# Kernel optimization log

Measured on AMD Instinct MI355X. Metric: run time of the kernel, lower is better.

## Reference

```python
import jax, jax.numpy as jnp
import numpy as np

B, N, F_IN, F_OUT = 16, 4096, 64, 64


def setup_inputs() -> dict:
    key = jax.random.key(0)
    k1, k2, k3, k4 = jax.random.split(key, 4)
    stdv = 1.0 / np.sqrt(F_OUT)
    graph = jax.random.normal(k1, (B, N, F_IN), dtype=jnp.float32)
    adj = jax.random.uniform(k2, (N, N), dtype=jnp.float32)
    weight = jax.random.uniform(k3, (F_IN, F_OUT), minval=-stdv, maxval=stdv, dtype=jnp.float32)
    bias = jax.random.uniform(k4, (F_OUT,), minval=-stdv, maxval=stdv, dtype=jnp.float32)
    return {"graph": graph, "adj": adj, "weight": weight, "bias": bias}


def _normalize_adj(adj):
    # Symmetric normalization D^{-1/2} A D^{-1/2}.
    # diag_embed @ adj @ diag_embed == row/col elementwise scaling (same math, O(N^2)).
    rowsum = jnp.sum(adj, axis=-1)
    rowsum = rowsum + (rowsum == 0).astype(adj.dtype)  # avoid div-by-zero for isolated nodes
    d_inv_sqrt = rowsum ** -0.5
    return d_inv_sqrt[:, None] * adj * d_inv_sqrt[None, :]


def reference(graph, adj, weight, bias):
    adj_norm = _normalize_adj(adj)                      # [N, N]
    support = jnp.einsum('bni,io->bno', graph, weight)  # [B, N, F_out]
    output = jnp.einsum('nm,bmo->bno', adj_norm, support)
    output = jax.nn.relu(output + bias)
    return (output, adj)
```

## Files before the change

kernel.cpp:

```cpp
#include <hip/hip_runtime.h>
#include <hip/hip_bf16.h>
#include <stdint.h>


typedef __bf16 bf16;
typedef __bf16 bf16x8 __attribute__((ext_vector_type(8)));
typedef float f32x4 __attribute__((ext_vector_type(4)));

#define NN 4096
#define BATCH 16
#define FD 64

__global__ __launch_bounds__(256) void k_prep(const float* __restrict__ adj,
                                              bf16* __restrict__ adjb,
                                              float* __restrict__ dsq) {
    int row = blockIdx.x;
    const float4* p = (const float4*)(adj + (size_t)row * NN);
    uint4* q = (uint4*)(adjb + (size_t)row * NN);
    float s = 0.f;
    for (int j = threadIdx.x; j < 512; j += 256) {
        float4 a = p[2 * j], b = p[2 * j + 1];
        bf16x8 h;
        h[0] = (bf16)a.x; h[1] = (bf16)a.y; h[2] = (bf16)a.z; h[3] = (bf16)a.w;
        h[4] = (bf16)b.x; h[5] = (bf16)b.y; h[6] = (bf16)b.z; h[7] = (bf16)b.w;
        q[j] = __builtin_bit_cast(uint4, h);
        s += a.x + a.y + a.z + a.w + b.x + b.y + b.z + b.w;
    }
    #pragma unroll
    for (int off = 32; off > 0; off >>= 1) s += __shfl_down(s, off, 64);
    __shared__ float red[4];
    int lane = threadIdx.x & 63, wv = threadIdx.x >> 6;
    if (lane == 0) red[wv] = s;
    __syncthreads();
    if (threadIdx.x == 0) {
        float t = red[0] + red[1] + red[2] + red[3];
        if (t == 0.f) t = 1.f;
        dsq[row] = 1.0f / sqrtf(t);
    }
}

__global__ __launch_bounds__(256) void k_support(const float* __restrict__ graph,
                                                 const float* __restrict__ weight,
                                                 const float* __restrict__ dsq,
                                                 bf16* __restrict__ spT) {
    __shared__ float wT[64 * 64];
    int tid = threadIdx.x;
    for (int idx = tid; idx < 4096; idx += 256) {
        int i = idx >> 6, o = idx & 63;
        wT[o * 64 + i] = weight[idx];
    }
    __syncthreads();
    int b = blockIdx.y;
    int m = blockIdx.x * 256 + tid;
    const float4* g4 = (const float4*)(graph + ((size_t)b * NN + m) * FD);
    float ds = dsq[m];
    float gr[64];
    #pragma unroll
    for (int j = 0; j < 16; j++) {
        float4 v = g4[j];
        gr[4 * j] = v.x * ds; gr[4 * j + 1] = v.y * ds;
        gr[4 * j + 2] = v.z * ds; gr[4 * j + 3] = v.w * ds;
    }
    bf16* outp = spT + m;
    for (int o = 0; o < 64; o++) {
        const float4* w4 = (const float4*)&wT[o * 64];
        float acc = 0.f;
        #pragma unroll
        for (int j = 0; j < 16; j++) {
            float4 wv = w4[j];
            acc += gr[4 * j] * wv.x + gr[4 * j + 1] * wv.y
                 + gr[4 * j + 2] * wv.z + gr[4 * j + 3] * wv.w;
        }
        outp[(size_t)(b * 64 + o) * NN] = (bf16)acc;
    }
}

__global__ __launch_bounds__(256) void k_gemm(const bf16* __restrict__ adjb,
                                              const bf16* __restrict__ spT,
                                              const float* __restrict__ dsq,
                                              const float* __restrict__ bias,
                                              float* __restrict__ out) {
    __shared__ uint4 lds_a[512];
    __shared__ uint4 lds_b[512];
    const int tid = threadIdx.x;
    const int lane = tid & 63;
    const int w = tid >> 6;
    const int n0 = blockIdx.x * 128;
    const int c0 = blockIdx.y * 128;

    const int q0 = tid, q1 = tid + 256;
    const uint4* pA0 = (const uint4*)(adjb + (size_t)(n0 + (q0 >> 2)) * NN) + (q0 & 3);
    const uint4* pA1 = (const uint4*)(adjb + (size_t)(n0 + (q1 >> 2)) * NN) + (q1 & 3);
    const uint4* pB0 = (const uint4*)(spT  + (size_t)(c0 + (q0 >> 2)) * NN) + (q0 & 3);
    const uint4* pB1 = (const uint4*)(spT  + (size_t)(c0 + (q1 >> 2)) * NN) + (q1 & 3);

    const int r = lane & 15, qo = lane >> 4;
    const int rm = (w >> 1) * 64, rc = (w & 1) * 64;
    const bf16x8* fA = (const bf16x8*)lds_a + (rm + r) * 4 + qo;
    const bf16x8* fB = (const bf16x8*)lds_b + (rc + r) * 4 + qo;

    f32x4 acc[4][4];
    #pragma unroll
    for (int i = 0; i < 4; i++)
        #pragma unroll
        for (int j = 0; j < 4; j++)
            acc[i][j] = (f32x4){0.f, 0.f, 0.f, 0.f};

    for (int kt = 0; kt < NN; kt += 32) {
        const int kd = kt >> 3;
        uint4 va0 = pA0[kd], va1 = pA1[kd];
        uint4 vb0 = pB0[kd], vb1 = pB1[kd];
        __syncthreads();
        lds_a[q0] = va0; lds_a[q1] = va1;
        lds_b[q0] = vb0; lds_b[q1] = vb1;
        __syncthreads();
        bf16x8 af[4], bfr[4];
        #pragma unroll
        for (int mi = 0; mi < 4; mi++) af[mi] = fA[mi * 64];
        #pragma unroll
        for (int ni = 0; ni < 4; ni++) bfr[ni] = fB[ni * 64];
        #pragma unroll
        for (int mi = 0; mi < 4; mi++)
            #pragma unroll
            for (int ni = 0; ni < 4; ni++)
                acc[mi][ni] = __builtin_amdgcn_mfma_f32_16x16x32_bf16(
                    af[mi], bfr[ni], acc[mi][ni], 0, 0, 0);
    }

    const int b_hi = (c0 + rc) >> 6;
    float* outp = out + (size_t)b_hi * (NN * FD);
    float bo[4];
    #pragma unroll
    for (int ni = 0; ni < 4; ni++) bo[ni] = bias[ni * 16 + r];
    #pragma unroll
    for (int mi = 0; mi < 4; mi++) {
        float dn[4];
        #pragma unroll
        for (int rr = 0; rr < 4; rr++) dn[rr] = dsq[n0 + rm + mi * 16 + qo * 4 + rr];
        #pragma unroll
        for (int ni = 0; ni < 4; ni++) {
            int o = ni * 16 + r;
            #pragma unroll
            for (int rr = 0; rr < 4; rr++) {
                int n = n0 + rm + mi * 16 + qo * 4 + rr;
                float v = fmaxf(dn[rr] * acc[mi][ni][rr] + bo[ni], 0.f);
                outp[(size_t)n * FD + o] = v;
            }
        }
    }
}

__global__ __launch_bounds__(256) void k_copy(const float4* __restrict__ src,
                                              float4* __restrict__ dst) {
    size_t i = (size_t)blockIdx.x * 256 + threadIdx.x;
    dst[i] = src[i];
}

extern "C" void kernel_launch(void* const* d_in, const int* in_sizes, int n_in,
                              void* d_out, int out_size, void* d_ws, size_t ws_size,
                              hipStream_t stream) {
    const float *graph = nullptr, *adj = nullptr, *weight = nullptr, *bias = nullptr;
    for (int i = 0; i < n_in; i++) {
        const float* p = (const float*)d_in[i];
        switch (in_sizes[i]) {
            case BATCH * NN * FD: graph  = p; break;
            case NN * NN:         adj    = p; break;
            case FD * FD:         weight = p; break;
            case FD:              bias   = p; break;
        }
    }

    float* out0 = (float*)d_out;
    float* out1 = out0 + (size_t)BATCH * NN * FD;

    const size_t off_spT = (size_t)NN * NN * 2;
    const size_t off_dsq = off_spT + (size_t)1024 * NN * 2;
    const size_t need    = off_dsq + (size_t)NN * 4;
    char* scratch = (ws_size >= need) ? (char*)d_ws : (char*)out1;
    bf16*  adjb = (bf16*)scratch;
    bf16*  spT  = (bf16*)(scratch + off_spT);
    float* dsq  = (float*)(scratch + off_dsq);

    hipLaunchKernelGGL(k_prep, dim3(NN), dim3(256), 0, stream, adj, adjb, dsq);
    hipLaunchKernelGGL(k_support, dim3(16, 16), dim3(256), 0, stream,
                       graph, weight, dsq, spT);
    hipLaunchKernelGGL(k_gemm, dim3(32, 8), dim3(256), 0, stream,
                       adjb, spT, dsq, bias, out0);
    hipLaunchKernelGGL(k_copy, dim3(16384), dim3(256), 0, stream,
                       (const float4*)adj, (float4*)out1);
}
```

Before: 266.8 us.

## Split-K GEMM with atomic accumulation, swizzled LDS, and fused adj copy

Splits the adjacency GEMM along K into 4 chunks. This raises the grid from 256 to 1024 blocks so the GPU's CUs are better filled, and each chunk's partials are added into a zeroed fp32 scratch buffer with atomics. A separate epilogue kernel then applies degree scaling, bias and ReLU. It also XOR-swizzles the LDS layout to cut bank conflicts, and folds the adj passthrough copy and accumulator zeroing into the prep kernel so the separate copy pass is skipped when workspace is available. The cost is 16MB of extra scratch traffic, atomic contention, and results that depend on the order of the atomic float adds.

```diff
diff --git a/kernel.cpp b/kernel.cpp
--- a/kernel.cpp
+++ b/kernel.cpp
@@ -10,22 +10,33 @@
 #define NN 4096
 #define BATCH 16
 #define FD 64
+#define CDIM 1024
+
+__device__ __forceinline__ int swz(int q) {
+    return (q & ~3) | ((q & 3) ^ ((q >> 3) & 3));
+}
 
 __global__ __launch_bounds__(256) void k_prep(const float* __restrict__ adj,
                                               bf16* __restrict__ adjb,
-                                              float* __restrict__ dsq) {
+                                              float* __restrict__ dsq,
+                                              float4* __restrict__ acc4,
+                                              float4* __restrict__ out1,
+                                              int do_copy) {
     int row = blockIdx.x;
     const float4* p = (const float4*)(adj + (size_t)row * NN);
     uint4* q = (uint4*)(adjb + (size_t)row * NN);
+    float4* o = out1 + (size_t)row * (NN / 4);
     float s = 0.f;
     for (int j = threadIdx.x; j < 512; j += 256) {
         float4 a = p[2 * j], b = p[2 * j + 1];
+        if (do_copy) { o[2 * j] = a; o[2 * j + 1] = b; }
         bf16x8 h;
         h[0] = (bf16)a.x; h[1] = (bf16)a.y; h[2] = (bf16)a.z; h[3] = (bf16)a.w;
         h[4] = (bf16)b.x; h[5] = (bf16)b.y; h[6] = (bf16)b.z; h[7] = (bf16)b.w;
         q[j] = __builtin_bit_cast(uint4, h);
         s += a.x + a.y + a.z + a.w + b.x + b.y + b.z + b.w;
     }
+    acc4[(size_t)row * 256 + threadIdx.x] = (float4){0.f, 0.f, 0.f, 0.f};
     #pragma unroll
     for (int off = 32; off > 0; off >>= 1) s += __shfl_down(s, off, 64);
     __shared__ float red[4];
@@ -77,9 +88,7 @@
 
 __global__ __launch_bounds__(256) void k_gemm(const bf16* __restrict__ adjb,
                                               const bf16* __restrict__ spT,
-                                              const float* __restrict__ dsq,
-                                              const float* __restrict__ bias,
-                                              float* __restrict__ out) {
+                                              float* __restrict__ accb) {
     __shared__ uint4 lds_a[512];
     __shared__ uint4 lds_b[512];
     const int tid = threadIdx.x;
@@ -87,32 +96,34 @@
     const int w = tid >> 6;
     const int n0 = blockIdx.x * 128;
     const int c0 = blockIdx.y * 128;
+    const size_t kbase = (size_t)blockIdx.z * (NN / 4);
 
     const int q0 = tid, q1 = tid + 256;
-    const uint4* pA0 = (const uint4*)(adjb + (size_t)(n0 + (q0 >> 2)) * NN) + (q0 & 3);
-    const uint4* pA1 = (const uint4*)(adjb + (size_t)(n0 + (q1 >> 2)) * NN) + (q1 & 3);
-    const uint4* pB0 = (const uint4*)(spT  + (size_t)(c0 + (q0 >> 2)) * NN) + (q0 & 3);
-    const uint4* pB1 = (const uint4*)(spT  + (size_t)(c0 + (q1 >> 2)) * NN) + (q1 & 3);
+    const int w0 = swz(q0), w1 = swz(q1);
+    const uint4* pA0 = (const uint4*)(adjb + (size_t)(n0 + (q0 >> 2)) * NN + kbase) + (q0 & 3);
+    const uint4* pA1 = (const uint4*)(adjb + (size_t)(n0 + (q1 >> 2)) * NN + kbase) + (q1 & 3);
+    const uint4* pB0 = (const uint4*)(spT  + (size_t)(c0 + (q0 >> 2)) * NN + kbase) + (q0 & 3);
+    const uint4* pB1 = (const uint4*)(spT  + (size_t)(c0 + (q1 >> 2)) * NN + kbase) + (q1 & 3);
 
     const int r = lane & 15, qo = lane >> 4;
     const int rm = (w >> 1) * 64, rc = (w & 1) * 64;
-    const bf16x8* fA = (const bf16x8*)lds_a + (rm + r) * 4 + qo;
-    const bf16x8* fB = (const bf16x8*)lds_b + (rc + r) * 4 + qo;
-
-    f32x4 acc[4][4];
+    const bf16x8* fA = (const bf16x8*)lds_a + (rm + r) * 4 + (qo ^ (((rm + r) >> 1) & 3));
+    const bf16x8* fB = (const bf16x8*)lds_b + (rc + r) * 4 + (qo ^ (((rc + r) >> 1) & 3));
+
+    f32x4 ac[4][4];
     #pragma unroll
     for (int i = 0; i < 4; i++)
         #pragma unroll
         for (int j = 0; j < 4; j++)
-            acc[i][j] = (f32x4){0.f, 0.f, 0.f, 0.f};
-
-    for (int kt = 0; kt < NN; kt += 32) {
+            ac[i][j] = (f32x4){0.f, 0.f, 0.f, 0.f};
+
+    for (int kt = 0; kt < NN / 4; kt += 32) {
         const int kd = kt >> 3;
         uint4 va0 = pA0[kd], va1 = pA1[kd];
         uint4 vb0 = pB0[kd], vb1 = pB1[kd];
         __syncthreads();
-        lds_a[q0] = va0; lds_a[q1] = va1;
-        lds_b[q0] = vb0; lds_b[q1] = vb1;
+        lds_a[w0] = va0; lds_a[w1] = va1;
+        lds_b[w0] = vb0; lds_b[w1] = vb1;
         __syncthreads();
         bf16x8 af[4], bfr[4];
         #pragma unroll
@@ -123,31 +134,40 @@
         for (int mi = 0; mi < 4; mi++)
             #pragma unroll
             for (int ni = 0; ni < 4; ni++)
-                acc[mi][ni] = __builtin_amdgcn_mfma_f32_16x16x32_bf16(
-                    af[mi], bfr[ni], acc[mi][ni], 0, 0, 0);
-    }
-
-    const int b_hi = (c0 + rc) >> 6;
-    float* outp = out + (size_t)b_hi * (NN * FD);
-    float bo[4];
-    #pragma unroll
-    for (int ni = 0; ni < 4; ni++) bo[ni] = bias[ni * 16 + r];
-    #pragma unroll
-    for (int mi = 0; mi < 4; mi++) {
-        float dn[4];
-        #pragma unroll
-        for (int rr = 0; rr < 4; rr++) dn[rr] = dsq[n0 + rm + mi * 16 + qo * 4 + rr];
+                ac[mi][ni] = __builtin_amdgcn_mfma_f32_16x16x32_bf16(
+                    af[mi], bfr[ni], ac[mi][ni], 0, 0, 0);
+    }
+
+    #pragma unroll
+    for (int mi = 0; mi < 4; mi++)
         #pragma unroll
         for (int ni = 0; ni < 4; ni++) {
-            int o = ni * 16 + r;
+            int c = c0 + rc + ni * 16 + r;
             #pragma unroll
             for (int rr = 0; rr < 4; rr++) {
                 int n = n0 + rm + mi * 16 + qo * 4 + rr;
-                float v = fmaxf(dn[rr] * acc[mi][ni][rr] + bo[ni], 0.f);
-                outp[(size_t)n * FD + o] = v;
+                unsafeAtomicAdd(&accb[(size_t)n * CDIM + c], ac[mi][ni][rr]);
             }
         }
-    }
+}
+
+__global__ __launch_bounds__(256) void k_epi(const float4* __restrict__ accv,
+                                             const float* __restrict__ dsq,
+                                             const float* __restrict__ bias,
+                                             float4* __restrict__ out0) {
+    int idx = blockIdx.x * 256 + threadIdx.x;
+    int flat = idx * 4;
+    int o4 = flat & 63;
+    int n = (flat >> 6) & (NN - 1);
+    int b = flat >> 18;
+    float4 a = accv[((size_t)n * CDIM + b * 64 + o4) >> 2];
+    float d = dsq[n];
+    float4 r;
+    r.x = fmaxf(a.x * d + bias[o4 + 0], 0.f);
+    r.y = fmaxf(a.y * d + bias[o4 + 1], 0.f);
+    r.z = fmaxf(a.z * d + bias[o4 + 2], 0.f);
+    r.w = fmaxf(a.w * d + bias[o4 + 3], 0.f);
+    out0[idx] = r;
 }
 
 __global__ __launch_bounds__(256) void k_copy(const float4* __restrict__ src,
@@ -174,18 +194,26 @@
     float* out1 = out0 + (size_t)BATCH * NN * FD;
 
     const size_t off_spT = (size_t)NN * NN * 2;
-    const size_t off_dsq = off_spT + (size_t)1024 * NN * 2;
-    const size_t need    = off_dsq + (size_t)NN * 4;
-    char* scratch = (ws_size >= need) ? (char*)d_ws : (char*)out1;
+    const size_t off_dsq = off_spT + (size_t)CDIM * NN * 2;
+    const size_t off_acc = off_dsq + (size_t)NN * 4;
+    const size_t need    = off_acc + (size_t)NN * CDIM * 4;
+    const int use_ws = (ws_size >= need);
+    char* scratch = use_ws ? (char*)d_ws : (char*)out1;
     bf16*  adjb = (bf16*)scratch;
     bf16*  spT  = (bf16*)(scratch + off_spT);
     float* dsq  = (float*)(scratch + off_dsq);
-
-    hipLaunchKernelGGL(k_prep, dim3(NN), dim3(256), 0, stream, adj, adjb, dsq);
+    float* accb = (float*)(scratch + off_acc);
+
+    hipLaunchKernelGGL(k_prep, dim3(NN), dim3(256), 0, stream,
+                       adj, adjb, dsq, (float4*)accb, (float4*)out1, use_ws);
     hipLaunchKernelGGL(k_support, dim3(16, 16), dim3(256), 0, stream,
                        graph, weight, dsq, spT);
-    hipLaunchKernelGGL(k_gemm, dim3(32, 8), dim3(256), 0, stream,
-                       adjb, spT, dsq, bias, out0);
-    hipLaunchKernelGGL(k_copy, dim3(16384), dim3(256), 0, stream,
-                       (const float4*)adj, (float4*)out1);
-}
+    hipLaunchKernelGGL(k_gemm, dim3(32, 8, 4), dim3(256), 0, stream,
+                       adjb, spT, accb);
+    hipLaunchKernelGGL(k_epi, dim3(4096), dim3(256), 0, stream,
+                       (const float4*)accb, dsq, bias, (float4*)out0);
+    if (!use_ws) {
+        hipLaunchKernelGGL(k_copy, dim3(16384), dim3(256), 0, stream,
+                           (const float4*)adj, (float4*)out1);
+    }
+}
```

New measurement: 281.1 us. 1.05x slower.
